# Kernel tuning notes

Hardware: AMD Instinct MI355X
Metric: run time of the kernel (lower is better)

The kernel has to match this reference:

```python
import jax, jax.numpy as jnp
import numpy as np

N, D, H = 262144, 512, 128


def _mlp(x, W1, b1, W2, b2):
    # Linear -> ReLU -> Linear
    return jax.nn.relu(x @ W1 + b1) @ W2 + b2


def setup_inputs() -> dict:
    key = jax.random.key(0)
    ks = jax.random.split(key, 8)
    features = jax.random.normal(ks[0], (N, D), dtype=jnp.float32)
    # last column is the routing flag: 0 -> transform expert, nonzero -> actor expert
    flags = jax.random.randint(ks[1], (N,), 0, 2).astype(jnp.float32)
    features = features.at[:, -1].set(flags)
    s = 0.02
    return {
        "features": features,
        "Wt1": jax.random.normal(ks[2], (D, H), dtype=jnp.float32) * s,
        "bt1": jnp.zeros((H,), dtype=jnp.float32),
        "Wt2": jax.random.normal(ks[3], (H, H), dtype=jnp.float32) * s,
        "bt2": jnp.zeros((H,), dtype=jnp.float32),
        "Wa1": jax.random.normal(ks[4], (D, H), dtype=jnp.float32) * s,
        "ba1": jnp.zeros((H,), dtype=jnp.float32),
        "Wa2": jax.random.normal(ks[5], (H, H), dtype=jnp.float32) * s,
        "ba2": jnp.zeros((H,), dtype=jnp.float32),
        "Wv1": jax.random.normal(ks[6], (D, H), dtype=jnp.float32) * s,
        "bv1": jnp.zeros((H,), dtype=jnp.float32),
        "Wv2": jax.random.normal(ks[7], (H, H), dtype=jnp.float32) * s,
        "bv2": jnp.zeros((H,), dtype=jnp.float32),
    }


def reference(features, Wt1, bt1, Wt2, bt2, Wa1, ba1, Wa2, ba2, Wv1, bv1, Wv2, bv2):
    # forward_actor: per-row dispatch on flag = features[:, -1]
    # flag == 0 -> policy_transform_net, else -> policy_actor_net.
    # Equivalent vectorized form: compute both experts, select per row.
    flag_is_zero = (features[:, -1] == 0)[:, None]  # [N, 1]
    trans_out = _mlp(features, Wt1, bt1, Wt2, bt2)   # [N, H]
    actor_out = _mlp(features, Wa1, ba1, Wa2, ba2)   # [N, H]
    latent_pi = jnp.where(flag_is_zero, trans_out, actor_out)
    # forward_critic: Linear-ReLU-Linear-ReLU
    latent_vf = jax.nn.relu(_mlp(features, Wv1, bv1, Wv2, bv2))
    return latent_pi, latent_vf
```

## Files before the change

kernel.cpp:

```cpp
#include <hip/hip_runtime.h>

#define NTOK 262144L

typedef __attribute__((ext_vector_type(4))) float f32x4;
typedef __attribute__((ext_vector_type(8))) short bf16x8;

static __device__ __forceinline__ unsigned short f2bf(float f) {
  unsigned int u = __builtin_bit_cast(unsigned int, f);
  u += 0x7fffu + ((u >> 16) & 1u);
  return (unsigned short)(u >> 16);
}

static __device__ __forceinline__ unsigned cvtpk(float lo, float hi) {
  unsigned r;
  asm("v_cvt_pk_bf16_f32 %0, %1, %2" : "=v"(r) : "v"(lo), "v"(hi));
  return r;
}

union U8 { unsigned u[4]; bf16x8 v; };

static __device__ __forceinline__ void dma16(const float* gsrc, void* ldst) {
  __builtin_amdgcn_global_load_lds(
      (const __attribute__((address_space(1))) unsigned int*)gsrc,
      (__attribute__((address_space(3))) unsigned int*)ldst, 16, 0, 0);
}

static __device__ __forceinline__ int sigx(int row) {
  return (row & 1) | ((row & 8) >> 2) | ((row & 6) << 2);
}
static __device__ __forceinline__ int swzh(int row) {
  return ((row & 8) << 1) | ((row & 6) << 5);
}

__global__ void pack_w(const float* __restrict__ Wt1, const float* __restrict__ Wa1,
                       const float* __restrict__ Wv1, const float* __restrict__ Wt2,
                       const float* __restrict__ Wa2, const float* __restrict__ Wv2,
                       unsigned short* __restrict__ pk) {
  int idx = blockIdx.x * 256 + threadIdx.x;
  if (idx >= 245760) return;
  float v;
  if (idx < 196608) {
    int j = idx & 7, l = (idx >> 3) & 63, ct = (idx >> 9) & 7, kt = (idx >> 12) & 15, e = idx >> 16;
    const float* W = (e == 0) ? Wt1 : (e == 1) ? Wa1 : Wv1;
    v = W[(kt * 32 + ((l >> 4) * 8) + j) * 128 + ct * 16 + (l & 15)];
  } else {
    int i2 = idx - 196608;
    int j = i2 & 7, l = (i2 >> 3) & 63, ct = (i2 >> 9) & 7, kt = (i2 >> 12) & 3, e = i2 >> 14;
    const float* W = (e == 0) ? Wt2 : (e == 1) ? Wa2 : Wv2;
    v = W[(kt * 32 + ((l >> 4) * 8) + j) * 128 + ct * 16 + (l & 15)];
  }
  pk[idx] = f2bf(v);
}

static __device__ __forceinline__ bf16x8 ldA(const char* xb, int row, int ktl, int g) {
  int swz = sigx(row) << 4;
  int base = row * 512 + ktl * 128 + g * 32;
  f32x4 f0 = *(const f32x4*)(xb + (base ^ swz));
  f32x4 f1 = *(const f32x4*)(xb + ((base + 16) ^ swz));
  U8 r;
  r.u[0] = cvtpk(f0[0], f0[1]);
  r.u[1] = cvtpk(f0[2], f0[3]);
  r.u[2] = cvtpk(f1[0], f1[1]);
  r.u[3] = cvtpk(f1[2], f1[3]);
  return r.v;
}

static __device__ __forceinline__ void stH(char* Hb, int g, int col, int rbase, f32x4 a) {
  #pragma unroll
  for (int rp = 0; rp < 2; ++rp) {
    int r0 = rbase + 4 * g + 2 * rp;
    unsigned p = cvtpk(fmaxf(a[2 * rp], 0.f), fmaxf(a[2 * rp + 1], 0.f));
    int a0 = r0 * 256 + ((((col >> 3) << 4)) ^ swzh(r0)) + (col & 7) * 2;
    int a1 = (r0 + 1) * 256 + ((((col >> 3) << 4)) ^ swzh(r0 + 1)) + (col & 7) * 2;
    *(unsigned short*)(Hb + a0) = (unsigned short)p;
    *(unsigned short*)(Hb + a1) = (unsigned short)(p >> 16);
  }
}

static __device__ __forceinline__ bf16x8 ldH(const char* hb, int row, int kt, int g) {
  return *(const bf16x8*)(hb + row * 256 + ((((kt * 4 + g) << 4)) ^ swzh(row)));
}

__global__ __launch_bounds__(256, 4) void mlp3(
    const float* __restrict__ X, const unsigned short* __restrict__ pk,
    const float* __restrict__ bt1, const float* __restrict__ bt2,
    const float* __restrict__ ba1, const float* __restrict__ ba2,
    const float* __restrict__ bv1, const float* __restrict__ bv2,
    float* __restrict__ out) {
  __shared__ float Xs[2 * 32 * 128];
  __shared__ unsigned short H0[32 * 128];
  __shared__ unsigned short H1[32 * 128];
  const int t = threadIdx.x;
  const long brow = (long)blockIdx.x * 32;
  const int lane = t & 63;
  const int w = t >> 6;
  const int l15 = lane & 15;
  const int g = lane >> 4;

  const float* __restrict__ Xrow = X + brow * 512;

  f32x4 at[2][2], aa[2][2], av[2][2];
  #pragma unroll
  for (int c = 0; c < 2; ++c) {
    float b0 = bt1[(2 * w + c) * 16 + l15];
    float b1v = ba1[(2 * w + c) * 16 + l15];
    float b2v = bv1[(2 * w + c) * 16 + l15];
    #pragma unroll
    for (int rt = 0; rt < 2; ++rt) {
      at[rt][c] = (f32x4){b0, b0, b0, b0};
      aa[rt][c] = (f32x4){b1v, b1v, b1v, b1v};
      av[rt][c] = (f32x4){b2v, b2v, b2v, b2v};
    }
  }

  #pragma unroll
  for (int i = 0; i < 4; ++i) {
    int lin = i * 256 + t;
    int row = lin >> 5, S = lin & 31;
    dma16(Xrow + row * 512 + ((S ^ sigx(row)) << 2),
          (char*)Xs + i * 4096 + w * 1024);
  }
  __syncthreads();

  unsigned fmask = 0;

  #pragma unroll
  for (int kc = 0; kc < 4; ++kc) {
    if (kc < 3) {
      #pragma unroll
      for (int i = 0; i < 4; ++i) {
        int lin = i * 256 + t;
        int row = lin >> 5, S = lin & 31;
        dma16(Xrow + row * 512 + (kc + 1) * 128 + ((S ^ sigx(row)) << 2),
              (char*)Xs + ((kc + 1) & 1) * 16384 + i * 4096 + w * 1024);
      }
    }
    const char* xb = (const char*)Xs + (kc & 1) * 16384;
    __builtin_amdgcn_s_setprio(1);
    #pragma unroll
    for (int ktl = 0; ktl < 4; ++ktl) {
      int kt = kc * 4 + ktl;
      int wo0 = ((kt * 8 + 2 * w) << 9) + (lane << 3);
      bf16x8 wt0 = *(const bf16x8*)(pk + wo0);
      bf16x8 wt1v = *(const bf16x8*)(pk + wo0 + 512);
      bf16x8 wa0 = *(const bf16x8*)(pk + 65536 + wo0);
      bf16x8 wa1v = *(const bf16x8*)(pk + 65536 + wo0 + 512);
      bf16x8 wv0 = *(const bf16x8*)(pk + 131072 + wo0);
      bf16x8 wv1v = *(const bf16x8*)(pk + 131072 + wo0 + 512);
      #pragma unroll
      for (int rt = 0; rt < 2; ++rt) {
        bf16x8 a = ldA(xb, rt * 16 + l15, ktl, g);
        at[rt][0] = __builtin_amdgcn_mfma_f32_16x16x32_bf16(a, wt0, at[rt][0], 0, 0, 0);
        at[rt][1] = __builtin_amdgcn_mfma_f32_16x16x32_bf16(a, wt1v, at[rt][1], 0, 0, 0);
        aa[rt][0] = __builtin_amdgcn_mfma_f32_16x16x32_bf16(a, wa0, aa[rt][0], 0, 0, 0);
        aa[rt][1] = __builtin_amdgcn_mfma_f32_16x16x32_bf16(a, wa1v, aa[rt][1], 0, 0, 0);
        av[rt][0] = __builtin_amdgcn_mfma_f32_16x16x32_bf16(a, wv0, av[rt][0], 0, 0, 0);
        av[rt][1] = __builtin_amdgcn_mfma_f32_16x16x32_bf16(a, wv1v, av[rt][1], 0, 0, 0);
      }
    }
    __builtin_amdgcn_s_setprio(0);
    if (kc == 3) {
      #pragma unroll
      for (int rt = 0; rt < 2; ++rt)
        #pragma unroll
        for (int r = 0; r < 4; ++r) {
          int row = rt * 16 + 4 * g + r;
          float fv = *(const float*)(xb + row * 512 + (((31 ^ sigx(row)) << 4)) + 12);
          if (fv != 0.f) fmask |= 1u << (rt * 4 + r);
        }
    }
    if (kc < 3) __syncthreads();
  }

  #pragma unroll
  for (int rt = 0; rt < 2; ++rt)
    #pragma unroll
    for (int c = 0; c < 2; ++c) {
      int col = (2 * w + c) * 16 + l15;
      stH((char*)H0, g, col, rt * 16, at[rt][c]);
      stH((char*)H1, g, col, rt * 16, aa[rt][c]);
    }
  __syncthreads();

  auto layer2 = [&](const unsigned short* Hb, int e, const float* __restrict__ b2, f32x4 a2[2][2]) {
    #pragma unroll
    for (int c = 0; c < 2; ++c) {
      float bv = b2[(2 * w + c) * 16 + l15];
      a2[0][c] = (f32x4){bv, bv, bv, bv};
      a2[1][c] = (f32x4){bv, bv, bv, bv};
    }
    const unsigned short* W2f = pk + 196608 + e * 16384;
    __builtin_amdgcn_s_setprio(1);
    #pragma unroll
    for (int kt = 0; kt < 4; ++kt) {
      int wo = ((kt * 8 + 2 * w) << 9) + (lane << 3);
      bf16x8 w0 = *(const bf16x8*)(W2f + wo);
      bf16x8 w1 = *(const bf16x8*)(W2f + wo + 512);
      #pragma unroll
      for (int rt = 0; rt < 2; ++rt) {
        bf16x8 a = ldH((const char*)Hb, rt * 16 + l15, kt, g);
        a2[rt][0] = __builtin_amdgcn_mfma_f32_16x16x32_bf16(a, w0, a2[rt][0], 0, 0, 0);
        a2[rt][1] = __builtin_amdgcn_mfma_f32_16x16x32_bf16(a, w1, a2[rt][1], 0, 0, 0);
      }
    }
    __builtin_amdgcn_s_setprio(0);
  };

  f32x4 keep[2][2], a2[2][2];
  layer2(H0, 0, bt2, keep);
  layer2(H1, 1, ba2, a2);
  #pragma unroll
  for (int rt = 0; rt < 2; ++rt)
    #pragma unroll
    for (int c = 0; c < 2; ++c)
      #pragma unroll
      for (int r = 0; r < 4; ++r)
        if ((fmask >> (rt * 4 + r)) & 1u) keep[rt][c][r] = a2[rt][c][r];
  __syncthreads();

  #pragma unroll
  for (int rt = 0; rt < 2; ++rt)
    #pragma unroll
    for (int c = 0; c < 2; ++c) {
      int col = (2 * w + c) * 16 + l15;
      stH((char*)H0, g, col, rt * 16, av[rt][c]);
    }
  __syncthreads();
  layer2(H0, 2, bv2, a2);

  float* __restrict__ ov = out + NTOK * 128;
  #pragma unroll
  for (int rt = 0; rt < 2; ++rt)
    #pragma unroll
    for (int c = 0; c < 2; ++c)
      #pragma unroll
      for (int r = 0; r < 4; ++r) {
        long row = brow + rt * 16 + 4 * g + r;
        long col = (2 * w + c) * 16 + l15;
        out[row * 128 + col] = keep[rt][c][r];
        ov[row * 128 + col] = fmaxf(a2[rt][c][r], 0.f);
      }
}

extern "C" void kernel_launch(void* const* d_in, const int* in_sizes, int n_in,
                              void* d_out, int out_size, void* d_ws, size_t ws_size,
                              hipStream_t stream) {
  const float* X   = (const float*)d_in[0];
  const float* Wt1 = (const float*)d_in[1];
  const float* bt1 = (const float*)d_in[2];
  const float* Wt2 = (const float*)d_in[3];
  const float* bt2 = (const float*)d_in[4];
  const float* Wa1 = (const float*)d_in[5];
  const float* ba1 = (const float*)d_in[6];
  const float* Wa2 = (const float*)d_in[7];
  const float* ba2 = (const float*)d_in[8];
  const float* Wv1 = (const float*)d_in[9];
  const float* bv1 = (const float*)d_in[10];
  const float* Wv2 = (const float*)d_in[11];
  const float* bv2 = (const float*)d_in[12];
  unsigned short* pk = (unsigned short*)d_ws;

  pack_w<<<960, 256, 0, stream>>>(Wt1, Wa1, Wv1, Wt2, Wa2, Wv2, pk);
  mlp3<<<8192, 256, 0, stream>>>(X, pk, bt1, bt2, ba1, ba2, bv1, bv2, (float*)d_out);
}
```

Baseline: 264.2 us.

## Load activations directly from global into registers, drop LDS staging

```diff
diff --git a/kernel.cpp b/kernel.cpp
--- a/kernel.cpp
+++ b/kernel.cpp
@@ -19,15 +19,6 @@
 
 union U8 { unsigned u[4]; bf16x8 v; };
 
-static __device__ __forceinline__ void dma16(const float* gsrc, void* ldst) {
-  __builtin_amdgcn_global_load_lds(
-      (const __attribute__((address_space(1))) unsigned int*)gsrc,
-      (__attribute__((address_space(3))) unsigned int*)ldst, 16, 0, 0);
-}
-
-static __device__ __forceinline__ int sigx(int row) {
-  return (row & 1) | ((row & 8) >> 2) | ((row & 6) << 2);
-}
 static __device__ __forceinline__ int swzh(int row) {
   return ((row & 8) << 1) | ((row & 6) << 5);
 }
@@ -52,19 +43,6 @@
   pk[idx] = f2bf(v);
 }
 
-static __device__ __forceinline__ bf16x8 ldA(const char* xb, int row, int ktl, int g) {
-  int swz = sigx(row) << 4;
-  int base = row * 512 + ktl * 128 + g * 32;
-  f32x4 f0 = *(const f32x4*)(xb + (base ^ swz));
-  f32x4 f1 = *(const f32x4*)(xb + ((base + 16) ^ swz));
-  U8 r;
-  r.u[0] = cvtpk(f0[0], f0[1]);
-  r.u[1] = cvtpk(f0[2], f0[3]);
-  r.u[2] = cvtpk(f1[0], f1[1]);
-  r.u[3] = cvtpk(f1[2], f1[3]);
-  return r.v;
-}
-
 static __device__ __forceinline__ void stH(char* Hb, int g, int col, int rbase, f32x4 a) {
   #pragma unroll
   for (int rp = 0; rp < 2; ++rp) {
@@ -87,9 +65,9 @@
     const float* __restrict__ ba1, const float* __restrict__ ba2,
     const float* __restrict__ bv1, const float* __restrict__ bv2,
     float* __restrict__ out) {
-  __shared__ float Xs[2 * 32 * 128];
   __shared__ unsigned short H0[32 * 128];
   __shared__ unsigned short H1[32 * 128];
+  __shared__ unsigned short H2[32 * 128];
   const int t = threadIdx.x;
   const long brow = (long)blockIdx.x * 32;
   const int lane = t & 63;
@@ -97,7 +75,14 @@
   const int l15 = lane & 15;
   const int g = lane >> 4;
 
-  const float* __restrict__ Xrow = X + brow * 512;
+  const float* __restrict__ A0 = X + (brow + l15) * 512 + g * 8;
+
+  float flg[8];
+  #pragma unroll
+  for (int rt = 0; rt < 2; ++rt)
+    #pragma unroll
+    for (int r = 0; r < 4; ++r)
+      flg[rt * 4 + r] = X[(brow + rt * 16 + 4 * g + r) * 512 + 511];
 
   f32x4 at[2][2], aa[2][2], av[2][2];
   #pragma unroll
@@ -113,63 +98,37 @@
     }
   }
 
-  #pragma unroll
-  for (int i = 0; i < 4; ++i) {
-    int lin = i * 256 + t;
-    int row = lin >> 5, S = lin & 31;
-    dma16(Xrow + row * 512 + ((S ^ sigx(row)) << 2),
-          (char*)Xs + i * 4096 + w * 1024);
-  }
-  __syncthreads();
-
-  unsigned fmask = 0;
-
-  #pragma unroll
-  for (int kc = 0; kc < 4; ++kc) {
-    if (kc < 3) {
-      #pragma unroll
-      for (int i = 0; i < 4; ++i) {
-        int lin = i * 256 + t;
-        int row = lin >> 5, S = lin & 31;
-        dma16(Xrow + row * 512 + (kc + 1) * 128 + ((S ^ sigx(row)) << 2),
-              (char*)Xs + ((kc + 1) & 1) * 16384 + i * 4096 + w * 1024);
-      }
-    }
-    const char* xb = (const char*)Xs + (kc & 1) * 16384;
-    __builtin_amdgcn_s_setprio(1);
-    #pragma unroll
-    for (int ktl = 0; ktl < 4; ++ktl) {
-      int kt = kc * 4 + ktl;
-      int wo0 = ((kt * 8 + 2 * w) << 9) + (lane << 3);
-      bf16x8 wt0 = *(const bf16x8*)(pk + wo0);
-      bf16x8 wt1v = *(const bf16x8*)(pk + wo0 + 512);
-      bf16x8 wa0 = *(const bf16x8*)(pk + 65536 + wo0);
-      bf16x8 wa1v = *(const bf16x8*)(pk + 65536 + wo0 + 512);
-      bf16x8 wv0 = *(const bf16x8*)(pk + 131072 + wo0);
-      bf16x8 wv1v = *(const bf16x8*)(pk + 131072 + wo0 + 512);
-      #pragma unroll
-      for (int rt = 0; rt < 2; ++rt) {
-        bf16x8 a = ldA(xb, rt * 16 + l15, ktl, g);
-        at[rt][0] = __builtin_amdgcn_mfma_f32_16x16x32_bf16(a, wt0, at[rt][0], 0, 0, 0);
-        at[rt][1] = __builtin_amdgcn_mfma_f32_16x16x32_bf16(a, wt1v, at[rt][1], 0, 0, 0);
-        aa[rt][0] = __builtin_amdgcn_mfma_f32_16x16x32_bf16(a, wa0, aa[rt][0], 0, 0, 0);
-        aa[rt][1] = __builtin_amdgcn_mfma_f32_16x16x32_bf16(a, wa1v, aa[rt][1], 0, 0, 0);
-        av[rt][0] = __builtin_amdgcn_mfma_f32_16x16x32_bf16(a, wv0, av[rt][0], 0, 0, 0);
-        av[rt][1] = __builtin_amdgcn_mfma_f32_16x16x32_bf16(a, wv1v, av[rt][1], 0, 0, 0);
-      }
-    }
-    __builtin_amdgcn_s_setprio(0);
-    if (kc == 3) {
-      #pragma unroll
-      for (int rt = 0; rt < 2; ++rt)
-        #pragma unroll
-        for (int r = 0; r < 4; ++r) {
-          int row = rt * 16 + 4 * g + r;
-          float fv = *(const float*)(xb + row * 512 + (((31 ^ sigx(row)) << 4)) + 12);
-          if (fv != 0.f) fmask |= 1u << (rt * 4 + r);
-        }
-    }
-    if (kc < 3) __syncthreads();
+  #pragma unroll 4
+  for (int kt = 0; kt < 16; ++kt) {
+    bf16x8 afr[2];
+    #pragma unroll
+    for (int rt = 0; rt < 2; ++rt) {
+      const float* p = A0 + rt * (16 * 512) + kt * 32;
+      f32x4 f0 = *(const f32x4*)p;
+      f32x4 f1 = *(const f32x4*)(p + 4);
+      U8 u;
+      u.u[0] = cvtpk(f0[0], f0[1]);
+      u.u[1] = cvtpk(f0[2], f0[3]);
+      u.u[2] = cvtpk(f1[0], f1[1]);
+      u.u[3] = cvtpk(f1[2], f1[3]);
+      afr[rt] = u.v;
+    }
+    const int wo = ((kt * 8 + 2 * w) << 9) + (lane << 3);
+    bf16x8 wt0 = *(const bf16x8*)(pk + wo);
+    bf16x8 wt1v = *(const bf16x8*)(pk + wo + 512);
+    bf16x8 wa0 = *(const bf16x8*)(pk + 65536 + wo);
+    bf16x8 wa1v = *(const bf16x8*)(pk + 65536 + wo + 512);
+    bf16x8 wv0 = *(const bf16x8*)(pk + 131072 + wo);
+    bf16x8 wv1v = *(const bf16x8*)(pk + 131072 + wo + 512);
+    #pragma unroll
+    for (int rt = 0; rt < 2; ++rt) {
+      at[rt][0] = __builtin_amdgcn_mfma_f32_16x16x32_bf16(afr[rt], wt0, at[rt][0], 0, 0, 0);
+      at[rt][1] = __builtin_amdgcn_mfma_f32_16x16x32_bf16(afr[rt], wt1v, at[rt][1], 0, 0, 0);
+      aa[rt][0] = __builtin_amdgcn_mfma_f32_16x16x32_bf16(afr[rt], wa0, aa[rt][0], 0, 0, 0);
+      aa[rt][1] = __builtin_amdgcn_mfma_f32_16x16x32_bf16(afr[rt], wa1v, aa[rt][1], 0, 0, 0);
+      av[rt][0] = __builtin_amdgcn_mfma_f32_16x16x32_bf16(afr[rt], wv0, av[rt][0], 0, 0, 0);
+      av[rt][1] = __builtin_amdgcn_mfma_f32_16x16x32_bf16(afr[rt], wv1v, av[rt][1], 0, 0, 0);
+    }
   }
 
   #pragma unroll
@@ -179,10 +138,12 @@
       int col = (2 * w + c) * 16 + l15;
       stH((char*)H0, g, col, rt * 16, at[rt][c]);
       stH((char*)H1, g, col, rt * 16, aa[rt][c]);
+      stH((char*)H2, g, col, rt * 16, av[rt][c]);
     }
   __syncthreads();
 
-  auto layer2 = [&](const unsigned short* Hb, int e, const float* __restrict__ b2, f32x4 a2[2][2]) {
+  auto layer2 = [&](const unsigned short* Hb, int e, const float* __restrict__ b2,
+                    f32x4 a2[2][2]) {
     #pragma unroll
     for (int c = 0; c < 2; ++c) {
       float bv = b2[(2 * w + c) * 16 + l15];
@@ -190,7 +151,6 @@
       a2[1][c] = (f32x4){bv, bv, bv, bv};
     }
     const unsigned short* W2f = pk + 196608 + e * 16384;
-    __builtin_amdgcn_s_setprio(1);
     #pragma unroll
     for (int kt = 0; kt < 4; ++kt) {
       int wo = ((kt * 8 + 2 * w) << 9) + (lane << 3);
@@ -203,7 +163,6 @@
         a2[rt][1] = __builtin_amdgcn_mfma_f32_16x16x32_bf16(a, w1, a2[rt][1], 0, 0, 0);
       }
     }
-    __builtin_amdgcn_s_setprio(0);
   };
 
   f32x4 keep[2][2], a2[2][2];
@@ -215,18 +174,8 @@
     for (int c = 0; c < 2; ++c)
       #pragma unroll
       for (int r = 0; r < 4; ++r)
-        if ((fmask >> (rt * 4 + r)) & 1u) keep[rt][c][r] = a2[rt][c][r];
-  __syncthreads();
-
-  #pragma unroll
-  for (int rt = 0; rt < 2; ++rt)
-    #pragma unroll
-    for (int c = 0; c < 2; ++c) {
-      int col = (2 * w + c) * 16 + l15;
-      stH((char*)H0, g, col, rt * 16, av[rt][c]);
-    }
-  __syncthreads();
-  layer2(H0, 2, bv2, a2);
+        if (flg[rt * 4 + r] != 0.f) keep[rt][c][r] = a2[rt][c][r];
+  layer2(H2, 2, bv2, a2);
 
   float* __restrict__ ov = out + NTOK * 128;
   #pragma unroll
```

After: 489.1 us. +85.1%, slower.
